# Kernel optimization log

Hardware: AMD Instinct MI355X
Metric: run time of the kernel (lower is better)

Reference implementation:

```python
import jax, jax.numpy as jnp
import numpy as np

B, N, M = 2, 2048, 2048
Q_DIM = 1024
HEADS = 8
DIM_HEAD = 64
INNER = HEADS * DIM_HEAD  # 512


def setup_inputs() -> dict:
    key = jax.random.key(0)
    ks = jax.random.split(key, 7)
    s_in = 1.0 / np.sqrt(Q_DIM)
    s_out = 1.0 / np.sqrt(INNER)
    return {
        "x": jax.random.normal(ks[0], (B, N, Q_DIM), dtype=jnp.float32),
        "context": jax.random.normal(ks[1], (B, M, Q_DIM), dtype=jnp.float32),
        "Wq": jax.random.normal(ks[2], (Q_DIM, INNER), dtype=jnp.float32) * s_in,
        "Wk": jax.random.normal(ks[3], (Q_DIM, INNER), dtype=jnp.float32) * s_in,
        "Wv": jax.random.normal(ks[4], (Q_DIM, INNER), dtype=jnp.float32) * s_in,
        "Wo": jax.random.normal(ks[5], (INNER, Q_DIM), dtype=jnp.float32) * s_out,
        "bo": jax.random.normal(ks[6], (Q_DIM,), dtype=jnp.float32) * 0.01,
    }


def reference(x, context, Wq, Wk, Wv, Wo, bo):
    scale = DIM_HEAD ** (-0.5)
    # projections, split heads: [b, n, inner] -> [b, h, n, d]
    def split_heads(t):
        b, n, _ = t.shape
        return t.reshape(b, n, HEADS, DIM_HEAD).transpose(0, 2, 1, 3)
    q = split_heads(x @ Wq)
    k = split_heads(context @ Wk)
    v = split_heads(context @ Wv)
    sim = jnp.einsum('bhid,bhjd->bhij', q, k) * scale  # [b,h,n,m] full score matrix
    attn = jax.nn.softmax(sim, axis=-1)
    out = jnp.einsum('bhij,bhjd->bhid', attn, v)       # [b,h,n,d]
    out = out.transpose(0, 2, 1, 3).reshape(x.shape[0], x.shape[1], INNER)
    return out @ Wo + bo
```

## Files before the change

### kernel.cpp

```cpp
#include <hip/hip_runtime.h>

typedef __attribute__((ext_vector_type(8))) short short8;
typedef __attribute__((ext_vector_type(4))) float floatx4;
typedef __attribute__((ext_vector_type(16))) float f32x16;
typedef __attribute__((ext_vector_type(4))) float f32x4;
typedef __attribute__((ext_vector_type(2))) unsigned uint2v;

__device__ __forceinline__ short f2bf(float f) {
    union { float f; unsigned u; } v;
    v.f = f;
    unsigned r = v.u + 0x7fffu + ((v.u >> 16) & 1u);
    return (short)(r >> 16);
}

#define MFMA_BF16(a, b, c) __builtin_amdgcn_mfma_f32_16x16x32_bf16((a), (b), (c), 0, 0, 0)
#define MFMA32(a, b, c)    __builtin_amdgcn_mfma_f32_32x32x16_bf16((a), (b), (c), 0, 0, 0)

__device__ __forceinline__ float fast_exp2(float x) {
#if __has_builtin(__builtin_amdgcn_exp2f)
    return __builtin_amdgcn_exp2f(x);
#else
    return exp2f(x);
#endif
}

__device__ __forceinline__ unsigned cvtpk(float lo, float hi) {
    unsigned r;
    asm("v_cvt_pk_bf16_f32 %0, %1, %2" : "=v"(r) : "v"(lo), "v"(hi));
    return r;
}

__device__ __forceinline__ void pl32(unsigned& a, unsigned& b) {
    asm("v_permlane32_swap_b32 %0, %1" : "+v"(a), "+v"(b));
}

__device__ __forceinline__ void gll16(const void* g, void* l) {
    __builtin_amdgcn_global_load_lds((const __attribute__((address_space(1))) void*)g,
                                     (__attribute__((address_space(3))) void*)l,
                                     16, 0, 0);
}

#define QSCALE_LOG2E 0.18033688011112042f

__global__ __launch_bounds__(256) void wfrag_all(const float* __restrict__ Wq,
                                                 const float* __restrict__ Wk,
                                                 const float* __restrict__ Wv,
                                                 const float* __restrict__ Wo,
                                                 short* __restrict__ WqF,
                                                 short* __restrict__ WkF,
                                                 short* __restrict__ WvF,
                                                 short* __restrict__ WoF) {
    const int z = blockIdx.y;
    const float* src = (z == 0) ? Wq : (z == 1) ? Wk : (z == 2) ? Wv : Wo;
    short* dst = (z == 0) ? WqF : (z == 1) ? WkF : (z == 2) ? WvF : WoF;
    const int nbits = (z < 3) ? 9 : 10;
    const int N = 1 << nbits;
    const int t = blockIdx.x * 256 + threadIdx.x;
    const int kb = t >> nbits;
    const int n = t & (N - 1);
    const float* s = src + (size_t)(kb * 8) * N + n;
    short8 v;
#pragma unroll
    for (int j = 0; j < 8; ++j) v[j] = f2bf(s[(size_t)j * N]);
    *(short8*)(dst + (size_t)t * 8) = v;
}

__global__ __launch_bounds__(256) void afrag(const float* __restrict__ x,
                                             const float* __restrict__ ctx,
                                             short* __restrict__ AxF,
                                             short* __restrict__ AcF) {
    const float* src = (blockIdx.z == 0) ? x : ctx;
    short* dst = (blockIdx.z == 0) ? AxF : AcF;
    const int r0 = blockIdx.x * 64;
    const int k0 = blockIdx.y * 64;
    __shared__ short tile[64][72];
    const int tid = threadIdx.x;
    {
        const int seg = tid & 15;
        const int rbase = tid >> 4;
#pragma unroll
        for (int i = 0; i < 4; ++i) {
            const int row = rbase + i * 16;
            f32x4 v = *(const f32x4*)(src + (size_t)(r0 + row) * 1024 + k0 + seg * 4);
            uint2v d;
            d[0] = cvtpk(v[0], v[1]);
            d[1] = cvtpk(v[2], v[3]);
            *(uint2v*)&tile[row][seg * 4] = d;
        }
    }
    __syncthreads();
    {
        const int kbl = tid >> 5;
        const int rbase = tid & 31;
#pragma unroll
        for (int j = 0; j < 2; ++j) {
            const int row = rbase + j * 32;
            short8 v = *(const short8*)(&tile[row][kbl * 8]);
            *(short8*)(dst + ((size_t)(k0 / 8 + kbl) * 4096 + r0 + row) * 8) = v;
        }
    }
}

__global__ __launch_bounds__(256, 3) void gemm_qkv(const short* __restrict__ AxF,
                                                   const short* __restrict__ AcF,
                                                   const short* __restrict__ WqF,
                                                   const short* __restrict__ WkF,
                                                   const short* __restrict__ WvF,
                                                   short* __restrict__ Qw,
                                                   short* __restrict__ Kw,
                                                   short* __restrict__ Vtw) {
    const int z = blockIdx.z;
    const short* AF = (z == 0) ? AxF : AcF;
    const short* WF = (z == 0) ? WqF : (z == 1) ? WkF : WvF;
    const int tid = threadIdx.x;
    const int w = tid >> 6;
    const int lane = tid & 63;
    const int quad = lane >> 4, ln = lane & 15;
    const int wr = w >> 1, wc = w & 1;
    const int row0 = blockIdx.x * 64;
    const int col0 = blockIdx.y * 128;

    const short* aBase = AF + ((size_t)quad * 4096 + row0 + wr * 32 + ln) * 8;
    const short* bBase = WF + ((size_t)quad * 512 + col0 + wc * 64 + ln) * 8;

    floatx4 acc[2][4] = {};
    short8 aR[4][2], bR[4][4];

    auto loadStep = [&](int it) {
        const int s = it & 3;
#pragma unroll
        for (int i = 0; i < 2; ++i)
            aR[s][i] = *(const short8*)(aBase + (size_t)it * 131072 + i * 128);
#pragma unroll
        for (int t = 0; t < 4; ++t)
            bR[s][t] = *(const short8*)(bBase + (size_t)it * 16384 + t * 128);
    };

    loadStep(0);
    loadStep(1);
    loadStep(2);
#pragma unroll
    for (int it = 0; it < 32; ++it) {
        if (it + 3 < 32) loadStep(it + 3);
        const int s = it & 3;
#pragma unroll
        for (int i = 0; i < 2; ++i)
#pragma unroll
            for (int t = 0; t < 4; ++t)
                acc[i][t] = MFMA_BF16(aR[s][i], bR[s][t], acc[i][t]);
    }

    const float oscale = (z == 0) ? QSCALE_LOG2E : 1.0f;
    short* dst = (z == 0) ? Qw : (z == 1) ? Kw : Vtw;
#pragma unroll
    for (int i = 0; i < 2; ++i)
#pragma unroll
        for (int t = 0; t < 4; ++t)
#pragma unroll
            for (int r = 0; r < 4; ++r) {
                const int R = row0 + wr * 32 + i * 16 + quad * 4 + r;
                const int C = col0 + wc * 64 + t * 16 + ln;
                const int b = R >> 11, n = R & 2047;
                const int h = C >> 6, d = C & 63;
                const short val = f2bf(acc[i][t][r] * oscale);
                if (z < 2)
                    dst[((b * 8 + h) * 2048 + n) * 64 + d] = val;
                else
                    dst[((b * 8 + h) * 64 + d) * 2048 + n] = val;
            }
}

__global__ __launch_bounds__(256, 2) void attn_kernel(const short* __restrict__ Q,
                                                      const short* __restrict__ K,
                                                      const short* __restrict__ Vt,
                                                      short* __restrict__ AwF) {
    const int tid = threadIdx.x;
    const int w = tid >> 6;
    const int lane = tid & 63;
    const int hi = lane >> 5;
    const int ln5 = lane & 31;

    const int L = blockIdx.x + 32 * blockIdx.y;
    const int xcd = L & 7, slot = L >> 3;
    const int bh = xcd * 2 + (slot >> 5);
    const int q0 = (slot & 31) * 64;

    __shared__ __align__(16) char smem[65536];
    char* const wbase = smem + w * 16384;

    const short* Qbh = Q + (size_t)bh * 2048 * 64;
    const char* kp = (const char*)(K + (size_t)bh * 2048 * 64);
    const char* vp = (const char*)(Vt + (size_t)bh * 64 * 2048);

    short8 qf[2][4];
#pragma unroll
    for (int qt = 0; qt < 2; ++qt)
#pragma unroll
        for (int ds = 0; ds < 4; ++ds)
            qf[qt][ds] = *(const short8*)(Qbh + (size_t)(q0 + qt * 32 + ln5) * 64 + ds * 16 + hi * 8);

    f32x16 O[2][2] = {};
    float lp0 = 0.f, lp1 = 0.f;

    const int lrow = lane >> 3, lu = lane & 7;
    const int swzK = ((lu ^ lrow) << 4);
    const int sw_r = (ln5 & 7) << 4;

    auto stageK = [&](int tile, int c) {
        char* kb = wbase + c * 8192;
#pragma unroll
        for (int i = 0; i < 4; ++i)
            gll16(kp + (size_t)tile * 4096 + (size_t)i * 1024 + lrow * 128 + swzK,
                  kb + i * 1024);
    };
    auto stageV = [&](int tile, int c) {
        char* vb = wbase + c * 8192 + 4096;
#pragma unroll
        for (int i = 0; i < 4; ++i) {
            const int u = lu ^ lrow;
            const int d = i * 8 + lrow + 32 * (u >> 2);
            gll16(vp + (size_t)d * 4096 + (size_t)tile * 64 + (u & 3) * 16,
                  vb + i * 1024);
        }
    };

    short8 PA[2][2];

    auto computeTile = [&](int c) {
        char* kb = wbase + c * 8192;
        char* vb = kb + 4096;
        short8 kf[4];
#pragma unroll
        for (int ds = 0; ds < 4; ++ds)
            kf[ds] = *(const short8*)(kb + ln5 * 128 + ((((ds * 2 + hi) << 4)) ^ sw_r));
        short8 vf[2][2];
#pragma unroll
        for (int dt = 0; dt < 2; ++dt)
#pragma unroll
            for (int k2 = 0; k2 < 2; ++k2)
                vf[dt][k2] = *(const short8*)(vb + ln5 * 128 +
                                              ((((dt * 4 + k2 * 2 + hi) << 4)) ^ sw_r));
        f32x16 s0 = {}, s1 = {};
        __builtin_amdgcn_s_setprio(1);
#pragma unroll
        for (int ds = 0; ds < 4; ++ds) {
            s0 = MFMA32(kf[ds], qf[0][ds], s0);
            s1 = MFMA32(kf[ds], qf[1][ds], s1);
        }
        __builtin_amdgcn_s_setprio(0);
        auto buildPA = [&](const f32x16& sv, float& lacc, short8& oA, short8& oB) {
            float p[16];
#pragma unroll
            for (int e = 0; e < 16; ++e) p[e] = fast_exp2(sv[e]);
            float t0 = 0.f, t1 = 0.f;
#pragma unroll
            for (int e = 0; e < 16; e += 2) { t0 += p[e]; t1 += p[e + 1]; }
            lacc += t0 + t1;
            unsigned c0 = cvtpk(p[0], p[1]),   c1 = cvtpk(p[2], p[3]);
            unsigned c2 = cvtpk(p[4], p[5]),   c3 = cvtpk(p[6], p[7]);
            unsigned c4 = cvtpk(p[8], p[9]),   c5 = cvtpk(p[10], p[11]);
            unsigned c6 = cvtpk(p[12], p[13]), c7 = cvtpk(p[14], p[15]);
            pl32(c0, c2); pl32(c1, c3);
            pl32(c4, c6); pl32(c5, c7);
            union U { short8 s8; unsigned u[4]; };
            U a; a.u[0] = c0; a.u[1] = c1; a.u[2] = c2; a.u[3] = c3; oA = a.s8;
            U b; b.u[0] = c4; b.u[1] = c5; b.u[2] = c6; b.u[3] = c7; oB = b.s8;
        };
        buildPA(s0, lp0, PA[0][0], PA[1][0]);
        buildPA(s1, lp1, PA[0][1], PA[1][1]);
        __builtin_amdgcn_s_setprio(1);
#pragma unroll
        for (int dt = 0; dt < 2; ++dt)
#pragma unroll
            for (int k2 = 0; k2 < 2; ++k2) {
                O[dt][0] = MFMA32(vf[dt][k2], PA[k2][0], O[dt][0]);
                O[dt][1] = MFMA32(vf[dt][k2], PA[k2][1], O[dt][1]);
            }
        __builtin_amdgcn_s_setprio(0);
    };

    stageK(w, 0);
    stageV(w, 0);
    int cur = 0;
    for (int t = 0; t < 16; ++t) {
        if (t < 15) {
            stageK(w + (t + 1) * 4, cur ^ 1);
            stageV(w + (t + 1) * 4, cur ^ 1);
            asm volatile("s_waitcnt vmcnt(8)" ::: "memory");
        } else {
            asm volatile("s_waitcnt vmcnt(0)" ::: "memory");
        }
        computeTile(cur);
        cur ^= 1;
    }
    __syncthreads();

    float* lpf = (float*)smem;
    {
        const float a = lp0 + __shfl_xor(lp0, 32);
        const float b = lp1 + __shfl_xor(lp1, 32);
        if (hi == 0) {
            lpf[w * 64 + ln5] = a;
            lpf[w * 64 + 32 + ln5] = b;
        }
    }
    __syncthreads();
    const int qq = tid & 63;
    const int k8a = tid >> 6;
    const float den = lpf[qq] + lpf[64 + qq] + lpf[128 + qq] + lpf[192 + qq];
    const float inv = 1.0f / den;
    __syncthreads();
    float* freg = (float*)smem + w * 4096;
#pragma unroll
    for (int dt = 0; dt < 2; ++dt)
#pragma unroll
        for (int qt = 0; qt < 2; ++qt)
#pragma unroll
            for (int e = 0; e < 16; ++e) {
                const int d = dt * 32 + (e & 3) + 8 * (e >> 2) + 4 * hi;
                freg[d * 64 + qt * 32 + ln5] = O[dt][qt][e];
            }
    __syncthreads();
    const int b = bh >> 3, h = bh & 7;
    const float* fall = (const float*)smem;
#pragma unroll
    for (int j = 0; j < 2; ++j) {
        const int k8 = k8a + j * 4;
        float a8[8];
#pragma unroll
        for (int dd = 0; dd < 8; ++dd) {
            const int d = k8 * 8 + dd;
            a8[dd] = fall[d * 64 + qq] + fall[4096 + d * 64 + qq] +
                     fall[8192 + d * 64 + qq] + fall[12288 + d * 64 + qq];
        }
        short8 o8;
#pragma unroll
        for (int dd = 0; dd < 8; ++dd) o8[dd] = f2bf(a8[dd] * inv);
        *(short8*)(AwF + ((size_t)(h * 8 + k8) * 4096 + (size_t)(b * 2048 + q0 + qq)) * 8) = o8;
    }
}

__global__ __launch_bounds__(256, 3) void gemm_final(const short* __restrict__ AwF,
                                                     const short* __restrict__ WoF,
                                                     const float* __restrict__ bias,
                                                     float* __restrict__ out) {
    const int tid = threadIdx.x;
    const int w = tid >> 6;
    const int lane = tid & 63;
    const int quad = lane >> 4, ln = lane & 15;
    const int wr = w >> 1, wc = w & 1;
    const int row0 = blockIdx.x * 64;
    const int col0 = blockIdx.y * 128;

    const short* aBase = AwF + ((size_t)quad * 4096 + row0 + wr * 32 + ln) * 8;
    const short* bBase = WoF + ((size_t)quad * 1024 + col0 + wc * 64 + ln) * 8;

    floatx4 acc[2][4] = {};
    short8 aR[4][2], bR[4][4];

    auto loadStep = [&](int it) {
        const int s = it & 3;
#pragma unroll
        for (int i = 0; i < 2; ++i)
            aR[s][i] = *(const short8*)(aBase + (size_t)it * 131072 + i * 128);
#pragma unroll
        for (int t = 0; t < 4; ++t)
            bR[s][t] = *(const short8*)(bBase + (size_t)it * 32768 + t * 128);
    };

    loadStep(0);
    loadStep(1);
    loadStep(2);
#pragma unroll
    for (int it = 0; it < 16; ++it) {
        if (it + 3 < 16) loadStep(it + 3);
        const int s = it & 3;
#pragma unroll
        for (int i = 0; i < 2; ++i)
#pragma unroll
            for (int t = 0; t < 4; ++t)
                acc[i][t] = MFMA_BF16(aR[s][i], bR[s][t], acc[i][t]);
    }

#pragma unroll
    for (int i = 0; i < 2; ++i)
#pragma unroll
        for (int t = 0; t < 4; ++t)
#pragma unroll
            for (int r = 0; r < 4; ++r) {
                const int R = row0 + wr * 32 + i * 16 + quad * 4 + r;
                const int C = col0 + wc * 64 + t * 16 + ln;
                out[(size_t)R * 1024 + C] = acc[i][t][r] + bias[C];
            }
}

extern "C" void kernel_launch(void* const* d_in, const int* in_sizes, int n_in,
                              void* d_out, int out_size, void* d_ws, size_t ws_size,
                              hipStream_t stream) {
    const float* x   = (const float*)d_in[0];
    const float* ctx = (const float*)d_in[1];
    const float* Wq  = (const float*)d_in[2];
    const float* Wk  = (const float*)d_in[3];
    const float* Wv  = (const float*)d_in[4];
    const float* Wo  = (const float*)d_in[5];
    const float* bo  = (const float*)d_in[6];
    float* out = (float*)d_out;

    char* ws = (char*)d_ws;
    size_t off = 0;
    auto alloc = [&](size_t bytes) { char* p = ws + off; off += (bytes + 255) & ~(size_t)255; return p; };

    short* WqF  = (short*)alloc(512 * 1024 * 2);
    short* WkF  = (short*)alloc(512 * 1024 * 2);
    short* WvF  = (short*)alloc(512 * 1024 * 2);
    short* WoF  = (short*)alloc(1024 * 512 * 2);
    short* AxF  = (short*)alloc((size_t)4096 * 1024 * 2);
    short* AcF  = (short*)alloc((size_t)4096 * 1024 * 2);
    short* Qw   = (short*)alloc((size_t)16 * 2048 * 64 * 2);
    short* Kw   = (short*)alloc((size_t)16 * 2048 * 64 * 2);
    short* Vtw  = (short*)alloc((size_t)16 * 2048 * 64 * 2);
    short* AwF  = (short*)alloc((size_t)4096 * 512 * 2);

    wfrag_all<<<dim3(256, 4), 256, 0, stream>>>(Wq, Wk, Wv, Wo, WqF, WkF, WvF, WoF);
    afrag<<<dim3(64, 16, 2), 256, 0, stream>>>(x, ctx, AxF, AcF);

    gemm_qkv<<<dim3(64, 4, 3), 256, 0, stream>>>(AxF, AcF, WqF, WkF, WvF, Qw, Kw, Vtw);

    attn_kernel<<<dim3(32, 16), 256, 0, stream>>>(Qw, Kw, Vtw, AwF);

    gemm_final<<<dim3(64, 8), 256, 0, stream>>>(AwF, WoF, bo, out);
}
```

Measured before the change: 156.6 us.

## Stage QKV and output GEMM tiles through double-buffered LDS with direct global-to-LDS loads

Both projection GEMMs stop loading MFMA fragments straight from global memory into per-wave register rings. Each block now cooperatively copies its A and B K-tiles into a double-buffered shared-memory area using direct global-to-LDS loads. Waves then read their fragments from LDS, so fragments shared by several waves are fetched from global memory only once. The cost is a block-wide barrier per K-tile, a shallower prefetch (one tile ahead instead of three steps), and about 48KB of LDS per block, with the occupancy hint of 3 blocks removed.

```diff
diff --git a/kernel.cpp b/kernel.cpp
--- a/kernel.cpp
+++ b/kernel.cpp
@@ -101,14 +101,14 @@
     }
 }
 
-__global__ __launch_bounds__(256, 3) void gemm_qkv(const short* __restrict__ AxF,
-                                                   const short* __restrict__ AcF,
-                                                   const short* __restrict__ WqF,
-                                                   const short* __restrict__ WkF,
-                                                   const short* __restrict__ WvF,
-                                                   short* __restrict__ Qw,
-                                                   short* __restrict__ Kw,
-                                                   short* __restrict__ Vtw) {
+__global__ __launch_bounds__(256) void gemm_qkv(const short* __restrict__ AxF,
+                                                const short* __restrict__ AcF,
+                                                const short* __restrict__ WqF,
+                                                const short* __restrict__ WkF,
+                                                const short* __restrict__ WvF,
+                                                short* __restrict__ Qw,
+                                                short* __restrict__ Kw,
+                                                short* __restrict__ Vtw) {
     const int z = blockIdx.z;
     const short* AF = (z == 0) ? AxF : AcF;
     const short* WF = (z == 0) ? WqF : (z == 1) ? WkF : WvF;
@@ -120,34 +120,55 @@
     const int row0 = blockIdx.x * 64;
     const int col0 = blockIdx.y * 128;
 
-    const short* aBase = AF + ((size_t)quad * 4096 + row0 + wr * 32 + ln) * 8;
-    const short* bBase = WF + ((size_t)quad * 512 + col0 + wc * 64 + ln) * 8;
+    __shared__ __align__(16) short lds[2][12288];
+
+    auto stage = [&](int buf, int kt) {
+        short* d = &lds[buf][0];
+        const int kb0 = kt * 8;
+#pragma unroll
+        for (int c = 0; c < 2; ++c) {
+            const int kb = c * 4 + w;
+            gll16(AF + ((size_t)(kb0 + kb) * 4096 + row0 + lane) * 8,
+                  d + kb * 512);
+        }
+#pragma unroll
+        for (int c = 0; c < 4; ++c) {
+            const int g = c * 4 + w;
+            const int kb = g >> 1, colb = (g & 1) * 64;
+            gll16(WF + ((size_t)(kb0 + kb) * 512 + col0 + colb + lane) * 8,
+                  d + 4096 + (kb * 128 + colb) * 8);
+        }
+    };
 
     floatx4 acc[2][4] = {};
-    short8 aR[4][2], bR[4][4];
-
-    auto loadStep = [&](int it) {
-        const int s = it & 3;
-#pragma unroll
-        for (int i = 0; i < 2; ++i)
-            aR[s][i] = *(const short8*)(aBase + (size_t)it * 131072 + i * 128);
-#pragma unroll
-        for (int t = 0; t < 4; ++t)
-            bR[s][t] = *(const short8*)(bBase + (size_t)it * 16384 + t * 128);
-    };
-
-    loadStep(0);
-    loadStep(1);
-    loadStep(2);
-#pragma unroll
-    for (int it = 0; it < 32; ++it) {
-        if (it + 3 < 32) loadStep(it + 3);
-        const int s = it & 3;
-#pragma unroll
-        for (int i = 0; i < 2; ++i)
-#pragma unroll
-            for (int t = 0; t < 4; ++t)
-                acc[i][t] = MFMA_BF16(aR[s][i], bR[s][t], acc[i][t]);
+
+    auto compute = [&](int buf) {
+        const short* sA = &lds[buf][0];
+        const short* sB = &lds[buf][4096];
+#pragma unroll
+        for (int s = 0; s < 2; ++s) {
+            const int kb = s * 4 + quad;
+            short8 aF[2], bF[4];
+#pragma unroll
+            for (int i = 0; i < 2; ++i)
+                aF[i] = *(const short8*)(sA + (kb * 64 + wr * 32 + i * 16 + ln) * 8);
+#pragma unroll
+            for (int j = 0; j < 4; ++j)
+                bF[j] = *(const short8*)(sB + (kb * 128 + wc * 64 + j * 16 + ln) * 8);
+#pragma unroll
+            for (int i = 0; i < 2; ++i)
+#pragma unroll
+                for (int j = 0; j < 4; ++j)
+                    acc[i][j] = MFMA_BF16(aF[i], bF[j], acc[i][j]);
+        }
+    };
+
+    stage(0, 0);
+    __syncthreads();
+    for (int t = 0; t < 16; ++t) {
+        if (t + 1 < 16) stage((t + 1) & 1, t + 1);
+        compute(t & 1);
+        __syncthreads();
     }
 
     const float oscale = (z == 0) ? QSCALE_LOG2E : 1.0f;
@@ -340,10 +361,10 @@
     }
 }
 
-__global__ __launch_bounds__(256, 3) void gemm_final(const short* __restrict__ AwF,
-                                                     const short* __restrict__ WoF,
-                                                     const float* __restrict__ bias,
-                                                     float* __restrict__ out) {
+__global__ __launch_bounds__(256) void gemm_final(const short* __restrict__ AwF,
+                                                  const short* __restrict__ WoF,
+                                                  const float* __restrict__ bias,
+                                                  float* __restrict__ out) {
     const int tid = threadIdx.x;
     const int w = tid >> 6;
     const int lane = tid & 63;
@@ -352,34 +373,55 @@
     const int row0 = blockIdx.x * 64;
     const int col0 = blockIdx.y * 128;
 
-    const short* aBase = AwF + ((size_t)quad * 4096 + row0 + wr * 32 + ln) * 8;
-    const short* bBase = WoF + ((size_t)quad * 1024 + col0 + wc * 64 + ln) * 8;
+    __shared__ __align__(16) short lds[2][12288];
+
+    auto stage = [&](int buf, int kt) {
+        short* d = &lds[buf][0];
+        const int kb0 = kt * 8;
+#pragma unroll
+        for (int c = 0; c < 2; ++c) {
+            const int kb = c * 4 + w;
+            gll16(AwF + ((size_t)(kb0 + kb) * 4096 + row0 + lane) * 8,
+                  d + kb * 512);
+        }
+#pragma unroll
+        for (int c = 0; c < 4; ++c) {
+            const int g = c * 4 + w;
+            const int kb = g >> 1, colb = (g & 1) * 64;
+            gll16(WoF + ((size_t)(kb0 + kb) * 1024 + col0 + colb + lane) * 8,
+                  d + 4096 + (kb * 128 + colb) * 8);
+        }
+    };
 
     floatx4 acc[2][4] = {};
-    short8 aR[4][2], bR[4][4];
-
-    auto loadStep = [&](int it) {
-        const int s = it & 3;
-#pragma unroll
-        for (int i = 0; i < 2; ++i)
-            aR[s][i] = *(const short8*)(aBase + (size_t)it * 131072 + i * 128);
-#pragma unroll
-        for (int t = 0; t < 4; ++t)
-            bR[s][t] = *(const short8*)(bBase + (size_t)it * 32768 + t * 128);
-    };
-
-    loadStep(0);
-    loadStep(1);
-    loadStep(2);
-#pragma unroll
-    for (int it = 0; it < 16; ++it) {
-        if (it + 3 < 16) loadStep(it + 3);
-        const int s = it & 3;
-#pragma unroll
-        for (int i = 0; i < 2; ++i)
-#pragma unroll
-            for (int t = 0; t < 4; ++t)
-                acc[i][t] = MFMA_BF16(aR[s][i], bR[s][t], acc[i][t]);
+
+    auto compute = [&](int buf) {
+        const short* sA = &lds[buf][0];
+        const short* sB = &lds[buf][4096];
+#pragma unroll
+        for (int s = 0; s < 2; ++s) {
+            const int kb = s * 4 + quad;
+            short8 aF[2], bF[4];
+#pragma unroll
+            for (int i = 0; i < 2; ++i)
+                aF[i] = *(const short8*)(sA + (kb * 64 + wr * 32 + i * 16 + ln) * 8);
+#pragma unroll
+            for (int j = 0; j < 4; ++j)
+                bF[j] = *(const short8*)(sB + (kb * 128 + wc * 64 + j * 16 + ln) * 8);
+#pragma unroll
+            for (int i = 0; i < 2; ++i)
+#pragma unroll
+                for (int j = 0; j < 4; ++j)
+                    acc[i][j] = MFMA_BF16(aF[i], bF[j], acc[i][j]);
+        }
+    };
+
+    stage(0, 0);
+    __syncthreads();
+    for (int t = 0; t < 8; ++t) {
+        if (t + 1 < 8) stage((t + 1) & 1, t + 1);
+        compute(t & 1);
+        __syncthreads();
     }
 
 #pragma unroll
```

Result: faster. 150.1 us (-4.1%).
